# Optimization experiments

Measured on AMD Instinct MI355X. Metric: run time of the kernel, lower is better.

## Reference

```python
import jax, jax.numpy as jnp
import numpy as np

N, E, D, R, G, C = 100000, 600000, 128, 4, 256, 16
EPS = 1e-5

def _rgcn(x, src, dst, edge_type, w_rel, w_root, b):
    # out_i = x_i @ W_root + b + sum_r mean_{j in N_r(i)} x_j @ W_r  (PyG RGCNConv, aggr='mean')
    x_src = x[src]                                   # [E, D] gather
    out = x @ w_root + b                             # [N, D]
    for r in range(R):
        m = (edge_type == r).astype(x.dtype)         # [E]
        msg = (x_src @ w_rel[r]) * m[:, None]        # [E, D]
        agg = jax.ops.segment_sum(msg, dst, num_segments=N)
        cnt = jax.ops.segment_sum(m, dst, num_segments=N)
        out = out + agg / jnp.maximum(cnt, 1.0)[:, None]
    return out

def _bn_eval(x, gamma, beta, mean, var):
    return (x - mean) * jax.lax.rsqrt(var + EPS) * gamma + beta

def setup_inputs() -> dict:
    key = jax.random.key(0)
    ks = jax.random.split(key, 12)
    x = jax.random.normal(ks[0], (N, D), dtype=jnp.float32)
    edge_index = jax.random.randint(ks[1], (2, E), 0, N)
    edge_type = jax.random.randint(ks[2], (E,), 0, R)
    batch = jnp.sort(jax.random.randint(ks[3], (N,), 0, G))
    s = 1.0 / np.sqrt(D)
    conv_rel_w = jax.random.normal(ks[4], (3, R, D, D), dtype=jnp.float32) * s
    conv_root_w = jax.random.normal(ks[5], (3, D, D), dtype=jnp.float32) * s
    conv_bias = jnp.zeros((3, D), dtype=jnp.float32)
    bn_gamma = jnp.ones((2, D), dtype=jnp.float32)
    bn_beta = jnp.zeros((2, D), dtype=jnp.float32)
    bn_mean = jax.random.normal(ks[6], (2, D), dtype=jnp.float32) * 0.1
    bn_var = jax.random.uniform(ks[7], (2, D), minval=0.5, maxval=1.5, dtype=jnp.float32)
    cls_w1 = jax.random.normal(ks[8], (D, D // 2), dtype=jnp.float32) * s
    cls_b1 = jnp.zeros((D // 2,), dtype=jnp.float32)
    cls_w2 = jax.random.normal(ks[9], (D // 2, C), dtype=jnp.float32) / np.sqrt(D // 2)
    cls_b2 = jnp.zeros((C,), dtype=jnp.float32)
    return {"x": x, "edge_index": edge_index, "edge_type": edge_type, "batch": batch,
            "conv_rel_w": conv_rel_w, "conv_root_w": conv_root_w, "conv_bias": conv_bias,
            "bn_gamma": bn_gamma, "bn_beta": bn_beta, "bn_mean": bn_mean, "bn_var": bn_var,
            "cls_w1": cls_w1, "cls_b1": cls_b1, "cls_w2": cls_w2, "cls_b2": cls_b2}

def reference(x, edge_index, edge_type, batch, conv_rel_w, conv_root_w, conv_bias,
              bn_gamma, bn_beta, bn_mean, bn_var, cls_w1, cls_b1, cls_w2, cls_b2):
    src, dst = edge_index[0], edge_index[1]
    prev = None
    h = x
    for i in range(3):
        h_new = _rgcn(h, src, dst, edge_type, conv_rel_w[i], conv_root_w[i], conv_bias[i])
        if prev is not None:
            h_new = h_new + prev  # residual (shapes always match: D==D)
        if i != 2:
            h_new = _bn_eval(h_new, bn_gamma[i], bn_beta[i], bn_mean[i], bn_var[i])
            h_new = jax.nn.elu(h_new)  # alpha=1; dropout inactive in eval
        prev = h_new
        h = h_new
    # global mean pool over graphs
    sums = jax.ops.segment_sum(h, batch, num_segments=G)          # [G, D]
    cnts = jax.ops.segment_sum(jnp.ones((N,), h.dtype), batch, num_segments=G)
    pooled = sums / jnp.maximum(cnts, 1.0)[:, None]
    z = jax.nn.elu(pooled @ cls_w1 + cls_b1)
    logits = z @ cls_w2 + cls_b2
    return jax.nn.log_softmax(logits, axis=-1)
```

## Files before the change

### kernel.cpp

```cpp
#include <hip/hip_runtime.h>
#include <hip/hip_bf16.h>

#define NN 100000
#define EE 600000
#define DD 128
#define GG 256
#define CCL 16

typedef __attribute__((ext_vector_type(8))) short short8;
typedef __attribute__((ext_vector_type(4))) float f32x4;
typedef const __attribute__((address_space(1))) void* gas_t;
typedef __attribute__((address_space(3))) void* las_t;

__device__ __forceinline__ void async_ld16(const void* g, void* l) {
    __builtin_amdgcn_global_load_lds((gas_t)g, (las_t)l, 16, 0, 0);
}
__device__ __forceinline__ unsigned short f2bf(float x) {
    unsigned u = __float_as_uint(x);
    unsigned r = (u + 0x7FFFu + ((u >> 16) & 1u)) >> 16;
    return (unsigned short)r;
}
__device__ __forceinline__ float bf2f(unsigned short b) {
    return __uint_as_float(((unsigned)b) << 16);
}
__device__ __forceinline__ void unpack8(uint4 v, float* f) {
    f[0] = __uint_as_float(v.x << 16); f[1] = __uint_as_float(v.x & 0xFFFF0000u);
    f[2] = __uint_as_float(v.y << 16); f[3] = __uint_as_float(v.y & 0xFFFF0000u);
    f[4] = __uint_as_float(v.z << 16); f[5] = __uint_as_float(v.z & 0xFFFF0000u);
    f[6] = __uint_as_float(v.w << 16); f[7] = __uint_as_float(v.w & 0xFFFF0000u);
}

__global__ __launch_bounds__(256) void sniff_kernel(const void* __restrict__ xraw, int* __restrict__ flag) {
    int t = threadIdx.x;
    const unsigned short* u = (const unsigned short*)xraw;
    int good = 0;
    #pragma unroll
    for (int i = 0; i < 4; i++) {
        unsigned short b = u[t * 4 + i];
        int e = (b >> 7) & 0xFF;
        if (e >= 107 && e <= 130) good++;
    }
    __shared__ int sg[256];
    sg[t] = good;
    __syncthreads();
    for (int s = 128; s > 0; s >>= 1) { if (t < s) sg[t] += sg[t + s]; __syncthreads(); }
    if (t == 0) flag[0] = (sg[0] >= 900) ? 1 : 0;
}

__device__ __forceinline__ float loadf(const void* p, size_t i, int isbf) {
    if (isbf) return bf2f(((const unsigned short*)p)[i]);
    return ((const float*)p)[i];
}

__global__ __launch_bounds__(256) void convx_kernel(const void* __restrict__ xraw, const int* __restrict__ flag,
                                                    __hip_bfloat16* __restrict__ xc) {
    int isbf = flag[0];
    size_t i0 = ((size_t)blockIdx.x * 256 + threadIdx.x) * 8;
    if (i0 >= (size_t)NN * DD) return;
    if (isbf) {
        *(uint4*)(xc + i0) = *(const uint4*)((const __hip_bfloat16*)xraw + i0);
    } else {
        const float* xf = (const float*)xraw;
        unsigned short o[8];
        #pragma unroll
        for (int j = 0; j < 8; j++) o[j] = f2bf(xf[i0 + j]);
        *(uint4*)(xc + i0) = *(uint4*)o;
    }
}

__global__ __launch_bounds__(256) void convw_kernel(const void* __restrict__ rel_raw, const void* __restrict__ root_raw,
                                                    const int* __restrict__ flag, __hip_bfloat16* __restrict__ wt) {
    int isbf = flag[0];
    int mat = blockIdx.x;
    int layer = mat / 5, g = mat % 5;
    size_t srcoff = (g == 0) ? (size_t)layer * 16384 : (size_t)(layer * 4 + (g - 1)) * 16384;
    const void* sraw = (g == 0) ? root_raw : rel_raw;
    __hip_bfloat16* dstp = wt + (size_t)mat * 16384;
    for (int idx = threadIdx.x; idx < 16384; idx += 256) {
        int k = idx >> 7, n = idx & 127;
        float v = loadf(sraw, srcoff + (size_t)k * 128 + n, isbf);
        dstp[n * 128 + k] = __float2bfloat16(v);
    }
}

__global__ __launch_bounds__(256) void convp_kernel(const void* bias, const void* bng, const void* bnb,
                                                    const void* bnm, const void* bnv, const void* w1,
                                                    const void* b1, const void* w2, const void* b2,
                                                    const int* __restrict__ flag, float* __restrict__ pf) {
    int isbf = flag[0];
    const void* srcs[9] = {bias, bng, bnb, bnm, bnv, w1, b1, w2, b2};
    const int cnts[9] = {384, 256, 256, 256, 256, 8192, 64, 1024, 16};
    const int offs[9] = {0, 384, 640, 896, 1152, 1408, 9600, 9664, 10688};
    int b = blockIdx.x;
    const void* s = srcs[b];
    int c = cnts[b], o = offs[b];
    for (int i = threadIdx.x; i < c; i += 256) pf[o + i] = loadf(s, i, isbf);
}

__global__ __launch_bounds__(256) void count4_kernel(const int* __restrict__ dst, const int* __restrict__ et,
                                                     int* __restrict__ cnt4) {
    int e = blockIdx.x * 256 + threadIdx.x;
    if (e < EE) atomicAdd(&cnt4[dst[e] * 4 + et[e]], 1);
}

__global__ __launch_bounds__(256) void alloc4_kernel(const int* __restrict__ cnt4, int* __restrict__ counter,
                                                     int* __restrict__ startp4, int* __restrict__ wptr4) {
    int wgid = blockIdx.x * 4 + (threadIdx.x >> 6);
    int lane = threadIdx.x & 63;
    int e0 = wgid * 256 + lane * 4;
    int4 cv = make_int4(0, 0, 0, 0);
    if (e0 < NN * 4) cv = *(const int4*)(cnt4 + e0);
    int c = cv.x + cv.y + cv.z + cv.w;
    int v = c;
    #pragma unroll
    for (int d = 1; d < 64; d <<= 1) {
        int o = __shfl_up(v, d);
        if (lane >= d) v += o;
    }
    int base = 0;
    if (lane == 63) base = atomicAdd(counter, v);
    base = __shfl(base, 63);
    if (e0 < NN * 4) {
        int s0 = base + v - c;
        int4 st;
        st.x = s0; st.y = s0 + cv.x; st.z = st.y + cv.y; st.w = st.z + cv.z;
        *(int4*)(startp4 + e0) = st;
        *(int4*)(wptr4 + e0) = st;
    }
}

__global__ __launch_bounds__(256) void fill4_kernel(const int* __restrict__ src, const int* __restrict__ dst,
                                                    const int* __restrict__ et, int* __restrict__ wptr4,
                                                    int* __restrict__ elist) {
    int e = blockIdx.x * 256 + threadIdx.x;
    if (e < EE) {
        int pos = atomicAdd(&wptr4[dst[e] * 4 + et[e]], 1);
        elist[pos] = src[e];
    }
}

__global__ __launch_bounds__(256) void agg_kernel(const __hip_bfloat16* __restrict__ h,
                                                  const int* __restrict__ elist,
                                                  const int* __restrict__ startp4,
                                                  const int* __restrict__ cnt4,
                                                  __hip_bfloat16* __restrict__ xagg) {
    int node = blockIdx.x * 16 + (threadIdx.x >> 4);
    int c16 = threadIdx.x & 15;
    const int* st = startp4 + node * 4;
    const int* cn = cnt4 + node * 4;
    __hip_bfloat16* outp = xagg + (size_t)node * 512;
    #pragma unroll
    for (int r = 0; r < 4; r++) {
        int s = st[r], c = cn[r];
        float a[8];
        #pragma unroll
        for (int j = 0; j < 8; j++) a[j] = 0.f;
        for (int i = 0; i < c; i++) {
            int srcn = elist[s + i];
            uint4 v = *(const uint4*)(h + (size_t)srcn * DD + c16 * 8);
            float f[8];
            unpack8(v, f);
            #pragma unroll
            for (int j = 0; j < 8; j++) a[j] += f[j];
        }
        float inv = 1.f / (float)(c > 0 ? c : 1);
        unsigned short u[8];
        #pragma unroll
        for (int j = 0; j < 8; j++) u[j] = f2bf(a[j] * inv);
        *(uint4*)(outp + r * 128 + c16 * 8) = *(uint4*)u;
    }
}

__global__ __launch_bounds__(256) void gemm_kernel(const __hip_bfloat16* __restrict__ h_in,
                                                   const __hip_bfloat16* __restrict__ xagg,
                                                   const __hip_bfloat16* __restrict__ wt,
                                                   const float* __restrict__ bias,
                                                   const float* __restrict__ bng,
                                                   const float* __restrict__ bnb,
                                                   const float* __restrict__ bnm,
                                                   const float* __restrict__ bnv,
                                                   const __hip_bfloat16* __restrict__ hres,
                                                   __hip_bfloat16* __restrict__ hout,
                                                   int do_bn) {
    __shared__ __align__(16) short lds[16384];
    __shared__ float sbias[128], sgm[128], sga[128];
    int t = threadIdx.x;
    int wave = t >> 6, lane = t & 63, quad = lane >> 4, r16 = lane & 15;
    int m0 = blockIdx.x * 128;

    if (t < 128) {
        sbias[t] = bias[t];
        float gm = 0.f, ga = 0.f;
        if (do_bn) {
            float iva = rsqrtf(bnv[t] + 1e-5f);
            gm = bng[t] * iva;
            ga = bnb[t] - bnm[t] * gm;
        }
        sgm[t] = gm; sga[t] = ga;
    }

    int r0 = m0 + wave * 32 + r16;      if (r0 > NN - 1) r0 = NN - 1;
    int r1 = m0 + wave * 32 + 16 + r16; if (r1 > NN - 1) r1 = NN - 1;

    f32x4 acc[2][8];
    #pragma unroll
    for (int i = 0; i < 2; i++)
        #pragma unroll
        for (int j = 0; j < 8; j++) acc[i][j] = (f32x4){0.f, 0.f, 0.f, 0.f};

    #pragma unroll
    for (int g = 0; g < 5; g++) {
        const __hip_bfloat16* wg = wt + (size_t)g * 16384;
        #pragma unroll
        for (int j = 0; j < 8; j++) {
            int slot = j * 256 + t;
            int row = slot >> 4, sp = slot & 15;
            int sg = sp ^ (row & 15);
            async_ld16(wg + row * 128 + sg * 8, &lds[slot * 8]);
        }
        __syncthreads();

        const __hip_bfloat16* a0p = (g == 0) ? (h_in + (size_t)r0 * 128)
                                             : (xagg + (size_t)r0 * 512 + (g - 1) * 128);
        const __hip_bfloat16* a1p = (g == 0) ? (h_in + (size_t)r1 * 128)
                                             : (xagg + (size_t)r1 * 512 + (g - 1) * 128);
        #pragma unroll
        for (int kc = 0; kc < 4; kc++) {
            short8 a0 = *(const short8*)(a0p + kc * 32 + quad * 8);
            short8 a1 = *(const short8*)(a1p + kc * 32 + quad * 8);
            int s = kc * 4 + quad;
            #pragma unroll
            for (int nt = 0; nt < 8; nt++) {
                int rb = nt * 16 + r16;
                short8 b = *(const short8*)&lds[(rb * 16 + (s ^ (rb & 15))) * 8];
                acc[0][nt] = __builtin_amdgcn_mfma_f32_16x16x32_bf16(a0, b, acc[0][nt], 0, 0, 0);
                acc[1][nt] = __builtin_amdgcn_mfma_f32_16x16x32_bf16(a1, b, acc[1][nt], 0, 0, 0);
            }
        }
        __syncthreads();
    }

    #pragma unroll
    for (int nt = 0; nt < 8; nt++) {
        int col = nt * 16 + r16;
        float bv = sbias[col];
        #pragma unroll
        for (int mt = 0; mt < 2; mt++) {
            #pragma unroll
            for (int reg = 0; reg < 4; reg++) {
                int row = wave * 32 + mt * 16 + quad * 4 + reg;
                int sslot = (col >> 3) ^ (row & 15);
                lds[row * 128 + sslot * 8 + (col & 7)] = (short)f2bf(acc[mt][nt][reg] + bv);
            }
        }
    }
    __syncthreads();
    int row = t >> 1, half = t & 1;
    int node = m0 + row;
    if (node < NN) {
        #pragma unroll
        for (int q = 0; q < 8; q++) {
            int seg = half * 8 + q;
            int sslot = seg ^ (row & 15);
            short8 cv = *(const short8*)&lds[row * 128 + sslot * 8];
            int col0 = seg * 8;
            float v[8];
            #pragma unroll
            for (int j = 0; j < 8; j++) v[j] = bf2f((unsigned short)cv[j]);
            if (hres) {
                float rf[8];
                unpack8(*(const uint4*)(hres + (size_t)node * 128 + col0), rf);
                #pragma unroll
                for (int j = 0; j < 8; j++) v[j] += rf[j];
            }
            if (do_bn) {
                #pragma unroll
                for (int j = 0; j < 8; j++) {
                    float z = v[j] * sgm[col0 + j] + sga[col0 + j];
                    v[j] = z > 0.f ? z : expm1f(z);
                }
            }
            unsigned short u[8];
            #pragma unroll
            for (int j = 0; j < 8; j++) u[j] = f2bf(v[j]);
            *(uint4*)(hout + (size_t)node * 128 + col0) = *(uint4*)u;
        }
    }
}

__global__ __launch_bounds__(256) void pool_kernel(const __hip_bfloat16* __restrict__ h3,
                                                   const int* __restrict__ batch,
                                                   float* __restrict__ pooled) {
    int g = blockIdx.x, t = threadIdx.x;
    int rowpar = t >> 4, colg = t & 15;
    int lo = 0, hi = NN;
    while (lo < hi) { int mid = (lo + hi) >> 1; if (batch[mid] < g) lo = mid + 1; else hi = mid; }
    int s0 = lo;
    hi = NN;
    while (lo < hi) { int mid = (lo + hi) >> 1; if (batch[mid] < g + 1) lo = mid + 1; else hi = mid; }
    int s1 = lo;
    float a[8];
    #pragma unroll
    for (int j = 0; j < 8; j++) a[j] = 0.f;
    for (int n = s0 + rowpar; n < s1; n += 16) {
        float f[8];
        unpack8(*(const uint4*)(h3 + (size_t)n * 128 + colg * 8), f);
        #pragma unroll
        for (int j = 0; j < 8; j++) a[j] += f[j];
    }
    __shared__ float sd[16][128];
    #pragma unroll
    for (int j = 0; j < 8; j++) sd[rowpar][colg * 8 + j] = a[j];
    __syncthreads();
    if (t < 128) {
        float sum = 0.f;
        #pragma unroll
        for (int i = 0; i < 16; i++) sum += sd[i][t];
        int cgn = s1 - s0;
        pooled[g * 128 + t] = sum / (float)(cgn > 0 ? cgn : 1);
    }
}

__global__ __launch_bounds__(64) void cls_kernel(const float* __restrict__ pooled,
                                                 const float* __restrict__ pf,
                                                 const int* __restrict__ flag,
                                                 void* __restrict__ out) {
    int g = blockIdx.x, j = threadIdx.x;
    const float* w1 = pf + 1408;
    const float* b1 = pf + 9600;
    const float* w2 = pf + 9664;
    const float* b2 = pf + 10688;
    __shared__ float z[64];
    __shared__ float lg[16];
    const float* p = pooled + g * 128;
    float acc = b1[j];
    for (int d = 0; d < 128; d++) acc += p[d] * w1[d * 64 + j];
    acc = acc > 0.f ? acc : expm1f(acc);
    z[j] = acc;
    __syncthreads();
    if (j < CCL) {
        float l = b2[j];
        for (int k = 0; k < 64; k++) l += z[k] * w2[k * 16 + j];
        lg[j] = l;
    }
    __syncthreads();
    if (j < CCL) {
        float m = lg[0];
        for (int k = 1; k < CCL; k++) m = fmaxf(m, lg[k]);
        float s = 0.f;
        for (int k = 0; k < CCL; k++) s += expf(lg[k] - m);
        float val = lg[j] - m - logf(s);
        if (flag[0]) ((__hip_bfloat16*)out)[g * CCL + j] = __float2bfloat16(val);
        else         ((float*)out)[g * CCL + j] = val;
    }
}

extern "C" void kernel_launch(void* const* d_in, const int* in_sizes, int n_in,
                              void* d_out, int out_size, void* d_ws, size_t ws_size,
                              hipStream_t stream) {
    const void* x_raw    = d_in[0];
    const int* ei        = (const int*)d_in[1];
    const int* et        = (const int*)d_in[2];
    const int* batch     = (const int*)d_in[3];
    const void* rel_raw  = d_in[4];
    const void* root_raw = d_in[5];
    const int* srcp = ei;
    const int* dstp = ei + EE;

    char* ws = (char*)d_ws;
    size_t off = 0;
    auto take = [&](size_t bytes) { size_t r = off; off += (bytes + 1023) & ~(size_t)1023; return r; };
    __hip_bfloat16* xagg = (__hip_bfloat16*)(ws + take((size_t)NN * 512 * 2));
    __hip_bfloat16* xc   = (__hip_bfloat16*)(ws + take((size_t)NN * 128 * 2));
    __hip_bfloat16* hA   = (__hip_bfloat16*)(ws + take((size_t)NN * 128 * 2));
    __hip_bfloat16* hB   = (__hip_bfloat16*)(ws + take((size_t)NN * 128 * 2));
    __hip_bfloat16* hC   = (__hip_bfloat16*)(ws + take((size_t)NN * 128 * 2));
    __hip_bfloat16* wt   = (__hip_bfloat16*)(ws + take((size_t)15 * 16384 * 2));
    float* pf            = (float*)(ws + take((size_t)10704 * 4));
    float* pooled        = (float*)(ws + take((size_t)GG * 128 * 4));
    int* cnt4            = (int*)(ws + take((size_t)NN * 16 + 8));
    int* counter         = cnt4 + NN * 4;
    int* flag            = cnt4 + NN * 4 + 1;
    int* startp4         = (int*)(ws + take((size_t)NN * 16));
    int* wptr4           = (int*)(ws + take((size_t)NN * 16));
    int* elist           = (int*)(ws + take((size_t)EE * 4));

    hipMemsetAsync(cnt4, 0, (size_t)NN * 16 + 4, stream);
    sniff_kernel<<<1, 256, 0, stream>>>(x_raw, flag);
    convx_kernel<<<(NN * DD / 8 + 255) / 256, 256, 0, stream>>>(x_raw, flag, xc);
    convw_kernel<<<15, 256, 0, stream>>>(rel_raw, root_raw, flag, wt);
    convp_kernel<<<9, 256, 0, stream>>>(d_in[6], d_in[7], d_in[8], d_in[9], d_in[10],
                                        d_in[11], d_in[12], d_in[13], d_in[14], flag, pf);
    count4_kernel<<<(EE + 255) / 256, 256, 0, stream>>>(dstp, et, cnt4);
    alloc4_kernel<<<(NN * 4 + 1023) / 1024, 256, 0, stream>>>(cnt4, counter, startp4, wptr4);
    fill4_kernel<<<(EE + 255) / 256, 256, 0, stream>>>(srcp, dstp, et, wptr4, elist);

    const __hip_bfloat16* hin = xc;
    __hip_bfloat16* houts[3] = {hA, hB, hC};
    for (int l = 0; l < 3; l++) {
        agg_kernel<<<NN / 16, 256, 0, stream>>>(hin, elist, startp4, cnt4, xagg);
        int bl = l < 2 ? l : 1;
        gemm_kernel<<<(NN + 127) / 128, 256, 0, stream>>>(
            hin, xagg, wt + (size_t)l * 5 * 16384, pf + l * 128,
            pf + 384 + bl * 128, pf + 640 + bl * 128, pf + 896 + bl * 128, pf + 1152 + bl * 128,
            (l > 0) ? hin : (const __hip_bfloat16*)nullptr, houts[l], (l < 2) ? 1 : 0);
        hin = houts[l];
    }
    pool_kernel<<<GG, 256, 0, stream>>>(houts[2], batch, pooled);
    cls_kernel<<<GG, 64, 0, stream>>>(pooled, pf, flag, (void*)d_out);
}
```

Measured before the change: 636.0 us.

## Fuse neighbor aggregation into RGCN GEMM kernel, dropping xagg buffer

```diff
diff --git a/kernel.cpp b/kernel.cpp
--- a/kernel.cpp
+++ b/kernel.cpp
@@ -139,40 +139,10 @@
     }
 }
 
-__global__ __launch_bounds__(256) void agg_kernel(const __hip_bfloat16* __restrict__ h,
-                                                  const int* __restrict__ elist,
-                                                  const int* __restrict__ startp4,
-                                                  const int* __restrict__ cnt4,
-                                                  __hip_bfloat16* __restrict__ xagg) {
-    int node = blockIdx.x * 16 + (threadIdx.x >> 4);
-    int c16 = threadIdx.x & 15;
-    const int* st = startp4 + node * 4;
-    const int* cn = cnt4 + node * 4;
-    __hip_bfloat16* outp = xagg + (size_t)node * 512;
-    #pragma unroll
-    for (int r = 0; r < 4; r++) {
-        int s = st[r], c = cn[r];
-        float a[8];
-        #pragma unroll
-        for (int j = 0; j < 8; j++) a[j] = 0.f;
-        for (int i = 0; i < c; i++) {
-            int srcn = elist[s + i];
-            uint4 v = *(const uint4*)(h + (size_t)srcn * DD + c16 * 8);
-            float f[8];
-            unpack8(v, f);
-            #pragma unroll
-            for (int j = 0; j < 8; j++) a[j] += f[j];
-        }
-        float inv = 1.f / (float)(c > 0 ? c : 1);
-        unsigned short u[8];
-        #pragma unroll
-        for (int j = 0; j < 8; j++) u[j] = f2bf(a[j] * inv);
-        *(uint4*)(outp + r * 128 + c16 * 8) = *(uint4*)u;
-    }
-}
-
-__global__ __launch_bounds__(256) void gemm_kernel(const __hip_bfloat16* __restrict__ h_in,
-                                                   const __hip_bfloat16* __restrict__ xagg,
+__global__ __launch_bounds__(256) void rgcn_kernel(const __hip_bfloat16* __restrict__ h_in,
+                                                   const int* __restrict__ elist,
+                                                   const int* __restrict__ startp4,
+                                                   const int* __restrict__ cnt4,
                                                    const __hip_bfloat16* __restrict__ wt,
                                                    const float* __restrict__ bias,
                                                    const float* __restrict__ bng,
@@ -182,87 +152,121 @@
                                                    const __hip_bfloat16* __restrict__ hres,
                                                    __hip_bfloat16* __restrict__ hout,
                                                    int do_bn) {
-    __shared__ __align__(16) short lds[16384];
-    __shared__ float sbias[128], sgm[128], sga[128];
+    __shared__ __align__(16) short Btile[16384];
+    __shared__ __align__(16) short Atile[8192];
+    __shared__ int ebuf[512];
+    __shared__ unsigned short srel[256], scnt[256];
+
     int t = threadIdx.x;
     int wave = t >> 6, lane = t & 63, quad = lane >> 4, r16 = lane & 15;
-    int m0 = blockIdx.x * 128;
-
-    if (t < 128) {
-        sbias[t] = bias[t];
-        float gm = 0.f, ga = 0.f;
-        if (do_bn) {
-            float iva = rsqrtf(bnv[t] + 1e-5f);
-            gm = bng[t] * iva;
-            ga = bnb[t] - bnm[t] * gm;
-        }
-        sgm[t] = gm; sga[t] = ga;
-    }
-
-    int r0 = m0 + wave * 32 + r16;      if (r0 > NN - 1) r0 = NN - 1;
-    int r1 = m0 + wave * 32 + 16 + r16; if (r1 > NN - 1) r1 = NN - 1;
-
-    f32x4 acc[2][8];
-    #pragma unroll
-    for (int i = 0; i < 2; i++)
-        #pragma unroll
-        for (int j = 0; j < 8; j++) acc[i][j] = (f32x4){0.f, 0.f, 0.f, 0.f};
+    int m0 = blockIdx.x * 64;
+
+    #pragma unroll
+    for (int j = 0; j < 8; j++) {
+        int slot = j * 256 + t;
+        int row = slot >> 4, sp = slot & 15;
+        async_ld16(wt + row * 128 + (sp ^ (row & 15)) * 8, &Btile[slot * 8]);
+    }
+    int e0 = startp4[m0 * 4];
+    int lastn = (m0 + 64 <= NN ? m0 + 64 : NN) - 1;
+    int ecount = startp4[lastn * 4 + 3] + cnt4[lastn * 4 + 3] - e0;
+    {
+        int gi = m0 * 4 + t;
+        int sr = 0, cv = 0;
+        if (gi < NN * 4) { sr = startp4[gi] - e0; cv = cnt4[gi]; }
+        srel[t] = (unsigned short)sr;
+        scnt[t] = (unsigned short)cv;
+    }
+    int ec2 = ecount < 512 ? ecount : 512;
+    for (int i = t; i < ec2; i += 256) ebuf[i] = elist[e0 + i];
+    #pragma unroll
+    for (int it = 0; it < 4; it++) {
+        int slot = it * 256 + t;
+        int row = slot >> 4, seg = slot & 15;
+        int node = m0 + row; if (node > NN - 1) node = NN - 1;
+        uint4 v = *(const uint4*)(h_in + (size_t)node * 128 + seg * 8);
+        *(uint4*)&Atile[(row * 16 + (seg ^ (row & 15))) * 8] = v;
+    }
+    __syncthreads();
+
+    f32x4 acc[8];
+    #pragma unroll
+    for (int j = 0; j < 8; j++) acc[j] = (f32x4){0.f, 0.f, 0.f, 0.f};
+
+    int grp = t >> 4, c16 = t & 15;
+    int arow = wave * 16 + r16;
 
     #pragma unroll
     for (int g = 0; g < 5; g++) {
-        const __hip_bfloat16* wg = wt + (size_t)g * 16384;
-        #pragma unroll
-        for (int j = 0; j < 8; j++) {
-            int slot = j * 256 + t;
-            int row = slot >> 4, sp = slot & 15;
-            int sg = sp ^ (row & 15);
-            async_ld16(wg + row * 128 + sg * 8, &lds[slot * 8]);
-        }
-        __syncthreads();
-
-        const __hip_bfloat16* a0p = (g == 0) ? (h_in + (size_t)r0 * 128)
-                                             : (xagg + (size_t)r0 * 512 + (g - 1) * 128);
-        const __hip_bfloat16* a1p = (g == 0) ? (h_in + (size_t)r1 * 128)
-                                             : (xagg + (size_t)r1 * 512 + (g - 1) * 128);
         #pragma unroll
         for (int kc = 0; kc < 4; kc++) {
-            short8 a0 = *(const short8*)(a0p + kc * 32 + quad * 8);
-            short8 a1 = *(const short8*)(a1p + kc * 32 + quad * 8);
+            short8 a = *(const short8*)&Atile[(arow * 16 + ((kc * 4 + quad) ^ (arow & 15))) * 8];
             int s = kc * 4 + quad;
             #pragma unroll
             for (int nt = 0; nt < 8; nt++) {
                 int rb = nt * 16 + r16;
-                short8 b = *(const short8*)&lds[(rb * 16 + (s ^ (rb & 15))) * 8];
-                acc[0][nt] = __builtin_amdgcn_mfma_f32_16x16x32_bf16(a0, b, acc[0][nt], 0, 0, 0);
-                acc[1][nt] = __builtin_amdgcn_mfma_f32_16x16x32_bf16(a1, b, acc[1][nt], 0, 0, 0);
+                short8 b = *(const short8*)&Btile[(rb * 16 + (s ^ (rb & 15))) * 8];
+                acc[nt] = __builtin_amdgcn_mfma_f32_16x16x32_bf16(a, b, acc[nt], 0, 0, 0);
             }
         }
         __syncthreads();
-    }
-
+        if (g < 4) {
+            const __hip_bfloat16* wg = wt + (size_t)(g + 1) * 16384;
+            #pragma unroll
+            for (int j = 0; j < 8; j++) {
+                int slot = j * 256 + t;
+                int row = slot >> 4, sp = slot & 15;
+                async_ld16(wg + row * 128 + (sp ^ (row & 15)) * 8, &Btile[slot * 8]);
+            }
+            #pragma unroll
+            for (int p = 0; p < 4; p++) {
+                int ni = p * 16 + grp;
+                int ni4 = ni * 4 + g;
+                int base = srel[ni4], c = scnt[ni4];
+                float a[8];
+                #pragma unroll
+                for (int j = 0; j < 8; j++) a[j] = 0.f;
+                for (int i = 0; i < c; i++) {
+                    int idx = base + i;
+                    int srcn = (idx < 512) ? ebuf[idx] : elist[e0 + idx];
+                    uint4 v = *(const uint4*)(h_in + (size_t)srcn * 128 + c16 * 8);
+                    float f[8];
+                    unpack8(v, f);
+                    #pragma unroll
+                    for (int j = 0; j < 8; j++) a[j] += f[j];
+                }
+                float inv = 1.f / (float)(c > 0 ? c : 1);
+                unsigned short u[8];
+                #pragma unroll
+                for (int j = 0; j < 8; j++) u[j] = f2bf(a[j] * inv);
+                *(uint4*)&Atile[(ni * 16 + (c16 ^ (ni & 15))) * 8] = *(uint4*)u;
+            }
+            __syncthreads();
+        }
+    }
+
+    __syncthreads();
+    short* Ctile = Atile;
     #pragma unroll
     for (int nt = 0; nt < 8; nt++) {
         int col = nt * 16 + r16;
-        float bv = sbias[col];
+        float bv = bias[col];
         #pragma unroll
-        for (int mt = 0; mt < 2; mt++) {
-            #pragma unroll
-            for (int reg = 0; reg < 4; reg++) {
-                int row = wave * 32 + mt * 16 + quad * 4 + reg;
-                int sslot = (col >> 3) ^ (row & 15);
-                lds[row * 128 + sslot * 8 + (col & 7)] = (short)f2bf(acc[mt][nt][reg] + bv);
-            }
+        for (int reg = 0; reg < 4; reg++) {
+            int row = wave * 16 + quad * 4 + reg;
+            int sslot = (col >> 3) ^ (row & 15);
+            Ctile[row * 128 + sslot * 8 + (col & 7)] = (short)f2bf(acc[nt][reg] + bv);
         }
     }
     __syncthreads();
-    int row = t >> 1, half = t & 1;
-    int node = m0 + row;
-    if (node < NN) {
-        #pragma unroll
-        for (int q = 0; q < 8; q++) {
-            int seg = half * 8 + q;
+    #pragma unroll
+    for (int it = 0; it < 4; it++) {
+        int u4 = it * 256 + t;
+        int row = u4 >> 4, seg = u4 & 15;
+        int node = m0 + row;
+        if (node < NN) {
             int sslot = seg ^ (row & 15);
-            short8 cv = *(const short8*)&lds[row * 128 + sslot * 8];
+            short8 cv = *(const short8*)&Ctile[row * 128 + sslot * 8];
             int col0 = seg * 8;
             float v[8];
             #pragma unroll
@@ -276,7 +280,10 @@
             if (do_bn) {
                 #pragma unroll
                 for (int j = 0; j < 8; j++) {
-                    float z = v[j] * sgm[col0 + j] + sga[col0 + j];
+                    int col = col0 + j;
+                    float iva = rsqrtf(bnv[col] + 1e-5f);
+                    float gm = bng[col] * iva;
+                    float z = v[j] * gm + (bnb[col] - bnm[col] * gm);
                     v[j] = z > 0.f ? z : expm1f(z);
                 }
             }
@@ -370,7 +377,6 @@
     char* ws = (char*)d_ws;
     size_t off = 0;
     auto take = [&](size_t bytes) { size_t r = off; off += (bytes + 1023) & ~(size_t)1023; return r; };
-    __hip_bfloat16* xagg = (__hip_bfloat16*)(ws + take((size_t)NN * 512 * 2));
     __hip_bfloat16* xc   = (__hip_bfloat16*)(ws + take((size_t)NN * 128 * 2));
     __hip_bfloat16* hA   = (__hip_bfloat16*)(ws + take((size_t)NN * 128 * 2));
     __hip_bfloat16* hB   = (__hip_bfloat16*)(ws + take((size_t)NN * 128 * 2));
@@ -398,10 +404,10 @@
     const __hip_bfloat16* hin = xc;
     __hip_bfloat16* houts[3] = {hA, hB, hC};
     for (int l = 0; l < 3; l++) {
-        agg_kernel<<<NN / 16, 256, 0, stream>>>(hin, elist, startp4, cnt4, xagg);
         int bl = l < 2 ? l : 1;
-        gemm_kernel<<<(NN + 127) / 128, 256, 0, stream>>>(
-            hin, xagg, wt + (size_t)l * 5 * 16384, pf + l * 128,
+        rgcn_kernel<<<(NN + 63) / 64, 256, 0, stream>>>(
+            hin, elist, startp4, cnt4,
+            wt + (size_t)l * 5 * 16384, pf + l * 128,
             pf + 384 + bl * 128, pf + 640 + bl * 128, pf + 896 + bl * 128, pf + 1152 + bl * 128,
             (l > 0) ? hin : (const __hip_bfloat16*)nullptr, houts[l], (l < 2) ? 1 : 0);
         hin = houts[l];
```

New measurement: 703.3 us. 1.11x slower.

## Split aggregation per relation segment and drop LDS weight staging in GEMM

Applied to the files above, without the earlier changes.

```diff
diff --git a/kernel.cpp b/kernel.cpp
--- a/kernel.cpp
+++ b/kernel.cpp
@@ -9,12 +9,7 @@
 
 typedef __attribute__((ext_vector_type(8))) short short8;
 typedef __attribute__((ext_vector_type(4))) float f32x4;
-typedef const __attribute__((address_space(1))) void* gas_t;
-typedef __attribute__((address_space(3))) void* las_t;
-
-__device__ __forceinline__ void async_ld16(const void* g, void* l) {
-    __builtin_amdgcn_global_load_lds((gas_t)g, (las_t)l, 16, 0, 0);
-}
+
 __device__ __forceinline__ unsigned short f2bf(float x) {
     unsigned u = __float_as_uint(x);
     unsigned r = (u + 0x7FFFu + ((u >> 16) & 1u)) >> 16;
@@ -144,31 +139,37 @@
                                                   const int* __restrict__ startp4,
                                                   const int* __restrict__ cnt4,
                                                   __hip_bfloat16* __restrict__ xagg) {
-    int node = blockIdx.x * 16 + (threadIdx.x >> 4);
+    int seg = blockIdx.x * 16 + (threadIdx.x >> 4);
     int c16 = threadIdx.x & 15;
-    const int* st = startp4 + node * 4;
-    const int* cn = cnt4 + node * 4;
-    __hip_bfloat16* outp = xagg + (size_t)node * 512;
-    #pragma unroll
-    for (int r = 0; r < 4; r++) {
-        int s = st[r], c = cn[r];
-        float a[8];
-        #pragma unroll
-        for (int j = 0; j < 8; j++) a[j] = 0.f;
-        for (int i = 0; i < c; i++) {
-            int srcn = elist[s + i];
-            uint4 v = *(const uint4*)(h + (size_t)srcn * DD + c16 * 8);
-            float f[8];
-            unpack8(v, f);
-            #pragma unroll
-            for (int j = 0; j < 8; j++) a[j] += f[j];
-        }
-        float inv = 1.f / (float)(c > 0 ? c : 1);
-        unsigned short u[8];
-        #pragma unroll
-        for (int j = 0; j < 8; j++) u[j] = f2bf(a[j] * inv);
-        *(uint4*)(outp + r * 128 + c16 * 8) = *(uint4*)u;
-    }
+    int s = startp4[seg], c = cnt4[seg];
+    float a[8];
+    #pragma unroll
+    for (int j = 0; j < 8; j++) a[j] = 0.f;
+    int i = 0;
+    for (; i + 2 <= c; i += 2) {
+        int s0 = elist[s + i], s1 = elist[s + i + 1];
+        uint4 v0 = *(const uint4*)(h + (size_t)s0 * DD + c16 * 8);
+        uint4 v1 = *(const uint4*)(h + (size_t)s1 * DD + c16 * 8);
+        float f0[8], f1[8];
+        unpack8(v0, f0);
+        unpack8(v1, f1);
+        #pragma unroll
+        for (int j = 0; j < 8; j++) a[j] += f0[j] + f1[j];
+    }
+    if (i < c) {
+        int s0 = elist[s + i];
+        uint4 v0 = *(const uint4*)(h + (size_t)s0 * DD + c16 * 8);
+        float f0[8];
+        unpack8(v0, f0);
+        #pragma unroll
+        for (int j = 0; j < 8; j++) a[j] += f0[j];
+    }
+    float inv = 1.f / (float)(c > 0 ? c : 1);
+    unsigned short u[8];
+    #pragma unroll
+    for (int j = 0; j < 8; j++) u[j] = f2bf(a[j] * inv);
+    int node = seg >> 2, r = seg & 3;
+    *(uint4*)(xagg + (size_t)node * 512 + r * 128 + c16 * 8) = *(uint4*)u;
 }
 
 __global__ __launch_bounds__(256) void gemm_kernel(const __hip_bfloat16* __restrict__ h_in,
@@ -182,87 +183,53 @@
                                                    const __hip_bfloat16* __restrict__ hres,
                                                    __hip_bfloat16* __restrict__ hout,
                                                    int do_bn) {
-    __shared__ __align__(16) short lds[16384];
-    __shared__ float sbias[128], sgm[128], sga[128];
+    __shared__ __align__(16) short Ctile[8192];
     int t = threadIdx.x;
     int wave = t >> 6, lane = t & 63, quad = lane >> 4, r16 = lane & 15;
-    int m0 = blockIdx.x * 128;
-
-    if (t < 128) {
-        sbias[t] = bias[t];
-        float gm = 0.f, ga = 0.f;
-        if (do_bn) {
-            float iva = rsqrtf(bnv[t] + 1e-5f);
-            gm = bng[t] * iva;
-            ga = bnb[t] - bnm[t] * gm;
-        }
-        sgm[t] = gm; sga[t] = ga;
-    }
-
-    int r0 = m0 + wave * 32 + r16;      if (r0 > NN - 1) r0 = NN - 1;
-    int r1 = m0 + wave * 32 + 16 + r16; if (r1 > NN - 1) r1 = NN - 1;
-
-    f32x4 acc[2][8];
-    #pragma unroll
-    for (int i = 0; i < 2; i++)
-        #pragma unroll
-        for (int j = 0; j < 8; j++) acc[i][j] = (f32x4){0.f, 0.f, 0.f, 0.f};
+    int m0 = blockIdx.x * 64;
+    int row = m0 + wave * 16 + r16;
+    if (row > NN - 1) row = NN - 1;
+
+    f32x4 acc[8];
+    #pragma unroll
+    for (int j = 0; j < 8; j++) acc[j] = (f32x4){0.f, 0.f, 0.f, 0.f};
 
     #pragma unroll
     for (int g = 0; g < 5; g++) {
+        const __hip_bfloat16* ap = (g == 0) ? (h_in + (size_t)row * 128)
+                                            : (xagg + (size_t)row * 512 + (g - 1) * 128);
         const __hip_bfloat16* wg = wt + (size_t)g * 16384;
         #pragma unroll
-        for (int j = 0; j < 8; j++) {
-            int slot = j * 256 + t;
-            int row = slot >> 4, sp = slot & 15;
-            int sg = sp ^ (row & 15);
-            async_ld16(wg + row * 128 + sg * 8, &lds[slot * 8]);
-        }
-        __syncthreads();
-
-        const __hip_bfloat16* a0p = (g == 0) ? (h_in + (size_t)r0 * 128)
-                                             : (xagg + (size_t)r0 * 512 + (g - 1) * 128);
-        const __hip_bfloat16* a1p = (g == 0) ? (h_in + (size_t)r1 * 128)
-                                             : (xagg + (size_t)r1 * 512 + (g - 1) * 128);
-        #pragma unroll
         for (int kc = 0; kc < 4; kc++) {
-            short8 a0 = *(const short8*)(a0p + kc * 32 + quad * 8);
-            short8 a1 = *(const short8*)(a1p + kc * 32 + quad * 8);
-            int s = kc * 4 + quad;
+            short8 a = *(const short8*)(ap + kc * 32 + quad * 8);
             #pragma unroll
             for (int nt = 0; nt < 8; nt++) {
-                int rb = nt * 16 + r16;
-                short8 b = *(const short8*)&lds[(rb * 16 + (s ^ (rb & 15))) * 8];
-                acc[0][nt] = __builtin_amdgcn_mfma_f32_16x16x32_bf16(a0, b, acc[0][nt], 0, 0, 0);
-                acc[1][nt] = __builtin_amdgcn_mfma_f32_16x16x32_bf16(a1, b, acc[1][nt], 0, 0, 0);
+                short8 b = *(const short8*)(wg + (nt * 16 + r16) * 128 + kc * 32 + quad * 8);
+                acc[nt] = __builtin_amdgcn_mfma_f32_16x16x32_bf16(a, b, acc[nt], 0, 0, 0);
             }
         }
-        __syncthreads();
     }
 
     #pragma unroll
     for (int nt = 0; nt < 8; nt++) {
         int col = nt * 16 + r16;
-        float bv = sbias[col];
-        #pragma unroll
-        for (int mt = 0; mt < 2; mt++) {
-            #pragma unroll
-            for (int reg = 0; reg < 4; reg++) {
-                int row = wave * 32 + mt * 16 + quad * 4 + reg;
-                int sslot = (col >> 3) ^ (row & 15);
-                lds[row * 128 + sslot * 8 + (col & 7)] = (short)f2bf(acc[mt][nt][reg] + bv);
-            }
+        float bv = bias[col];
+        #pragma unroll
+        for (int reg = 0; reg < 4; reg++) {
+            int crow = wave * 16 + quad * 4 + reg;
+            int sslot = (col >> 3) ^ (crow & 15);
+            Ctile[crow * 128 + sslot * 8 + (col & 7)] = (short)f2bf(acc[nt][reg] + bv);
         }
     }
     __syncthreads();
-    int row = t >> 1, half = t & 1;
-    int node = m0 + row;
-    if (node < NN) {
-        #pragma unroll
-        for (int q = 0; q < 8; q++) {
-            int seg = half * 8 + q;
-            int sslot = seg ^ (row & 15);
-            short8 cv = *(const short8*)&lds[row * 128 + sslot * 8];
+    #pragma unroll
+    for (int it = 0; it < 4; it++) {
+        int u4 = it * 256 + t;
+        int crow = u4 >> 4, seg = u4 & 15;
+        int node = m0 + crow;
+        if (node < NN) {
+            int sslot = seg ^ (crow & 15);
+            short8 cv = *(const short8*)&Ctile[crow * 128 + sslot * 8];
             int col0 = seg * 8;
             float v[8];
             #pragma unroll
@@ -276,7 +243,10 @@
             if (do_bn) {
                 #pragma unroll
                 for (int j = 0; j < 8; j++) {
-                    float z = v[j] * sgm[col0 + j] + sga[col0 + j];
+                    int col = col0 + j;
+                    float iva = rsqrtf(bnv[col] + 1e-5f);
+                    float gm = bng[col] * iva;
+                    float z = v[j] * gm + (bnb[col] - bnm[col] * gm);
                     v[j] = z > 0.f ? z : expm1f(z);
                 }
             }
@@ -398,9 +368,9 @@
     const __hip_bfloat16* hin = xc;
     __hip_bfloat16* houts[3] = {hA, hB, hC};
     for (int l = 0; l < 3; l++) {
-        agg_kernel<<<NN / 16, 256, 0, stream>>>(hin, elist, startp4, cnt4, xagg);
+        agg_kernel<<<(NN * 4) / 16, 256, 0, stream>>>(hin, elist, startp4, cnt4, xagg);
         int bl = l < 2 ? l : 1;
-        gemm_kernel<<<(NN + 127) / 128, 256, 0, stream>>>(
+        gemm_kernel<<<(NN + 63) / 64, 256, 0, stream>>>(
             hin, xagg, wt + (size_t)l * 5 * 16384, pf + l * 128,
             pf + 384 + bl * 128, pf + 640 + bl * 128, pf + 896 + bl * 128, pf + 1152 + bl * 128,
             (l > 0) ? hin : (const __hip_bfloat16*)nullptr, houts[l], (l < 2) ? 1 : 0);
```

After: 1.015 ms. 1.6x slower.
